# Kernel optimization log

Hardware: AMD Instinct MI355X
Metric: run time of the kernel (lower is better)

The kernel has to match this reference:

```python
import jax, jax.numpy as jnp
import numpy as np

N, IN, OUT, H = 8192, 128, 64, 4
NEG_SLOPE = 0.2   # GATConv leaky-relu slope
EPS = 1e-5        # BatchNorm1d eps
MASK_VAL = -1e9   # masked_fill value for non-edges (finite for grad safety)


def setup_inputs() -> dict:
    key = jax.random.key(0)
    ks = jax.random.split(key, 5)
    x = jax.random.normal(ks[0], (N, IN), jnp.float32)
    adj = jax.random.randint(ks[1], (N, N), 0, 2, jnp.int32)  # dense 0/1 adjacency
    W = jax.random.normal(ks[2], (H, IN, OUT), jnp.float32) * (1.0 / np.sqrt(IN))
    a_i = jax.random.normal(ks[3], (H, OUT), jnp.float32) * (1.0 / np.sqrt(OUT))
    a_j = jax.random.normal(ks[4], (H, OUT), jnp.float32) * (1.0 / np.sqrt(OUT))
    gamma = jnp.ones((H * OUT,), jnp.float32)   # BN weight
    beta = jnp.zeros((H * OUT,), jnp.float32)   # BN bias
    return {"x": x, "adj": adj, "W": W, "a_i": a_i, "a_j": a_j,
            "gamma": gamma, "beta": beta}


def reference(x, adj, W, a_i, a_j, gamma, beta):
    # --- GATConv (dense adjacency, multi-head, concat) ---
    h = jnp.einsum('ni,hio->hno', x, W)              # [H, N, OUT]
    ei = jnp.einsum('hno,ho->hn', h, a_i)            # [H, N] source scores
    ej = jnp.einsum('hno,ho->hn', h, a_j)            # [H, N] target scores
    coe = ei[:, :, None] + ej[:, None, :]            # [H, N, N]
    coe = jnp.where(coe >= 0, coe, NEG_SLOPE * coe)  # leaky_relu
    coe = jnp.where(adj[None, :, :] == 0, MASK_VAL, coe)
    att = jax.nn.softmax(coe, axis=-1)               # segment softmax over neighbors
    out = jnp.einsum('hnm,hmo->hno', att, h)         # weighted aggregation
    out = jnp.transpose(out, (1, 0, 2)).reshape(N, H * OUT)  # concat heads
    # --- BatchNorm1d (training-mode batch stats over nodes) ---
    mean = jnp.mean(out, axis=0)
    var = jnp.var(out, axis=0)
    out = (out - mean) * jax.lax.rsqrt(var + EPS) * gamma + beta
    # --- ReLU ---
    return jax.nn.relu(out)
```

## Files before the change

kernel.cpp:

```cpp
#include <hip/hip_runtime.h>
#include <hip/hip_bf16.h>

#define NN   8192
#define IND  128
#define OUTD 64
#define NH   4
#define NEG_SLOPE 0.2f
#define BN_EPS 1e-5f

typedef __attribute__((ext_vector_type(8))) short bf16x8;
typedef __attribute__((ext_vector_type(4))) float f32x4;
typedef __attribute__((ext_vector_type(4))) int   i32x4;

static __device__ __forceinline__ short f2bf(float f) {
    union { float f; unsigned u; } v; v.f = f;
    return (short)((v.u + 0x8000u) >> 16);
}

__global__ __launch_bounds__(256) void k0_repackW(const float* __restrict__ W,
                                                  short* __restrict__ WB) {
    int tid = blockIdx.x * 256 + threadIdx.x;
    int o = tid & 63, i = (tid >> 6) & 127, h = tid >> 13;
    WB[((h * 16 + (i >> 3)) * 64 + o) * 8 + (i & 7)] = f2bf(W[(h * 128 + i) * 64 + o]);
}

__global__ __launch_bounds__(256) void k1_feat(const float* __restrict__ x,
                                               const short* __restrict__ WB,
                                               const float* __restrict__ a_i,
                                               const float* __restrict__ a_j,
                                               short* __restrict__ hB,
                                               float* __restrict__ t_ei,  float* __restrict__ t_Ri,
                                               float* __restrict__ t_nj,
                                               float* __restrict__ t_E1j, float* __restrict__ t_E2j) {
    int w = threadIdx.x >> 6;
    int l = threadIdx.x & 63;
    int quad = l >> 4, lx = l & 15;
    int rb = blockIdx.x;

    f32x4 acc[4] = {};
#pragma unroll
    for (int ks = 0; ks < 4; ++ks) {
        const float* xp = x + (rb * 16 + lx) * IND + ks * 32 + quad * 8;
        f32x4 xa = *(const f32x4*)xp;
        f32x4 xb = *(const f32x4*)(xp + 4);
        bf16x8 af;
#pragma unroll
        for (int j = 0; j < 4; ++j) { af[j] = f2bf(xa[j]); af[4 + j] = f2bf(xb[j]); }
#pragma unroll
        for (int ot = 0; ot < 4; ++ot) {
            bf16x8 bf = *(const bf16x8*)(WB + ((w * 16 + ks * 4 + quad) * 64 + ot * 16 + lx) * 8);
            acc[ot] = __builtin_amdgcn_mfma_f32_16x16x32_bf16(af, bf, acc[ot], 0, 0, 0);
        }
    }
    float aiv[4], ajv[4];
#pragma unroll
    for (int ot = 0; ot < 4; ++ot) {
        aiv[ot] = a_i[w * 64 + ot * 16 + lx];
        ajv[ot] = a_j[w * 64 + ot * 16 + lx];
    }
#pragma unroll
    for (int reg = 0; reg < 4; ++reg) {
        int row = rb * 16 + quad * 4 + reg;
        float ei = 0.f, ej = 0.f;
#pragma unroll
        for (int ot = 0; ot < 4; ++ot) {
            float hv = acc[ot][reg];
            ei += hv * aiv[ot];
            ej += hv * ajv[ot];
        }
#pragma unroll
        for (int m = 1; m <= 8; m <<= 1) {
            ei += __shfl_xor(ei, m, 64);
            ej += __shfl_xor(ej, m, 64);
        }
        if (lx == reg) {
            t_ei [w * NN + row] = ei;
            t_Ri [w * NN + row] = expf(-0.8f * ei);
            t_nj [w * NN + row] = -ej;
            t_E1j[w * NN + row] = expf(ej);
            t_E2j[w * NN + row] = expf(NEG_SLOPE * ej);
        }
#pragma unroll
        for (int ot = 0; ot < 4; ++ot) {
            int o = ot * 16 + lx;
            hB[((w * 1024 + (row >> 3)) * 64 + o) * 8 + (row & 7)] = f2bf(acc[ot][reg]);
        }
    }
}

__global__ __launch_bounds__(256) void k2_attn(const int* __restrict__ adj,
                                               const short* __restrict__ hB,
                                               const float* __restrict__ t_ei,
                                               const float* __restrict__ t_Ri,
                                               const float* __restrict__ t_nj,
                                               const float* __restrict__ t_E1j,
                                               const float* __restrict__ t_E2j,
                                               float* __restrict__ num,
                                               float* __restrict__ Lsum) {
    __shared__ unsigned char smask[64 * 260];
    int tid = threadIdx.x;
    int w = tid >> 6;
    int l = tid & 63;
    int quad = l >> 4, lx = l & 15;
    int rb = blockIdx.x >> 2, ks = blockIdx.x & 3;
    int rowbase = rb * 64;
    int tb = w * NN;
    int k0 = ks * 2048;

    {
        int kc = tid * 8;
#pragma unroll 2
        for (int i = 0; i < 64; ++i) {
            const int* ap = adj + (size_t)(rowbase + i) * NN + k0 + kc;
            i32x4 a0 = *(const i32x4*)ap;
            i32x4 a1 = *(const i32x4*)(ap + 4);
            unsigned m = 0;
#pragma unroll
            for (int j = 0; j < 4; ++j) {
                m |= (a0[j] ? 1u : 0u) << j;
                m |= (a1[j] ? 1u : 0u) << (4 + j);
            }
            smask[i * 260 + tid] = (unsigned char)m;
        }
    }
    __syncthreads();

    float eiv[4], Riv[4];
    int mrow[4];
#pragma unroll
    for (int r = 0; r < 4; ++r) {
        int i = rowbase + r * 16 + lx;
        eiv[r] = t_ei[tb + i];
        Riv[r] = t_Ri[tb + i];
        mrow[r] = (r * 16 + lx) * 260 + quad;
    }

    bf16x8 onesf;
#pragma unroll
    for (int j = 0; j < 8; ++j) onesf[j] = (short)0x3F80;

    f32x4 acc[4][4] = {};
    f32x4 accL[4] = {};
    f32x4 pnj0, pnj1, pe10, pe11, pe20, pe21;
    {
        int kb = k0 + quad * 8;
        pnj0 = *(const f32x4*)(t_nj  + tb + kb);
        pnj1 = *(const f32x4*)(t_nj  + tb + kb + 4);
        pe10 = *(const f32x4*)(t_E1j + tb + kb);
        pe11 = *(const f32x4*)(t_E1j + tb + kb + 4);
        pe20 = *(const f32x4*)(t_E2j + tb + kb);
        pe21 = *(const f32x4*)(t_E2j + tb + kb + 4);
    }

#pragma unroll 1
    for (int kt = 0; kt < 64; ++kt) {
        f32x4 nj0 = pnj0, nj1 = pnj1;
        f32x4 e1j0 = pe10, e1j1 = pe11;
        f32x4 e2j0 = pe20, e2j1 = pe21;
        int mc[4];
#pragma unroll
        for (int r = 0; r < 4; ++r) mc[r] = smask[mrow[r] + kt * 4];

        int ktn = (kt + 1) & 63;
        int kbn = k0 + ktn * 32 + quad * 8;
        pnj0 = *(const f32x4*)(t_nj  + tb + kbn);
        pnj1 = *(const f32x4*)(t_nj  + tb + kbn + 4);
        pe10 = *(const f32x4*)(t_E1j + tb + kbn);
        pe11 = *(const f32x4*)(t_E1j + tb + kbn + 4);
        pe20 = *(const f32x4*)(t_E2j + tb + kbn);
        pe21 = *(const f32x4*)(t_E2j + tb + kbn + 4);

        int kb = k0 + kt * 32 + quad * 8;
        bf16x8 bfrag[4];
#pragma unroll
        for (int ot = 0; ot < 4; ++ot)
            bfrag[ot] = *(const bf16x8*)(hB + ((w * 1024 + (kb >> 3)) * 64 + ot * 16 + lx) * 8);

        bf16x8 afr[4];
#pragma unroll
        for (int r = 0; r < 4; ++r) {
            union { i32x4 i; bf16x8 b; } af;
#pragma unroll
            for (int jj = 0; jj < 4; ++jj) {
                int j0 = 2 * jj, j1 = 2 * jj + 1;
                float njA = (j0 < 4) ? nj0[j0] : nj1[j0 - 4];
                float njB = (j1 < 4) ? nj0[j1] : nj1[j1 - 4];
                float e1A = (j0 < 4) ? e1j0[j0] : e1j1[j0 - 4];
                float e1B = (j1 < 4) ? e1j0[j1] : e1j1[j1 - 4];
                float e2A = (j0 < 4) ? e2j0[j0] : e2j1[j0 - 4];
                float e2B = (j1 < 4) ? e2j0[j1] : e2j1[j1 - 4];
                float p0 = (eiv[r] >= njA) ? e1A : Riv[r] * e2A;
                float p1 = (eiv[r] >= njB) ? e1B : Riv[r] * e2B;
                p0 = (mc[r] & (1 << j0)) ? p0 : 0.0f;
                p1 = (mc[r] & (1 << j1)) ? p1 : 0.0f;
                af.i[jj] = (int)__builtin_amdgcn_perm(__float_as_uint(p1),
                                                      __float_as_uint(p0),
                                                      0x07060302);
            }
            afr[r] = af.b;
        }
#pragma unroll
        for (int r = 0; r < 4; ++r)
            accL[r] = __builtin_amdgcn_mfma_f32_16x16x32_bf16(afr[r], onesf, accL[r], 0, 0, 0);
#pragma unroll
        for (int r = 0; r < 4; ++r)
#pragma unroll
            for (int ot = 0; ot < 4; ++ot)
                acc[r][ot] = __builtin_amdgcn_mfma_f32_16x16x32_bf16(afr[r], bfrag[ot], acc[r][ot], 0, 0, 0);
    }

#pragma unroll
    for (int r = 0; r < 4; ++r)
        if (lx == 0)
#pragma unroll
            for (int reg = 0; reg < 4; ++reg)
                atomicAdd(&Lsum[w * NN + rowbase + r * 16 + quad * 4 + reg], accL[r][reg]);
#pragma unroll
    for (int r = 0; r < 4; ++r)
#pragma unroll
        for (int ot = 0; ot < 4; ++ot)
#pragma unroll
            for (int reg = 0; reg < 4; ++reg) {
                int row = rowbase + r * 16 + quad * 4 + reg;
                atomicAdd(&num[row * 256 + w * 64 + ot * 16 + lx], acc[r][ot][reg]);
            }
}

__global__ __launch_bounds__(256) void k3_combine(float* __restrict__ num,
                                                  const float* __restrict__ Lsum,
                                                  float* __restrict__ stats) {
    int c = threadIdx.x;
    int h = c >> 6;
    float s = 0.f, s2 = 0.f;
#pragma unroll
    for (int rr = 0; rr < 8; ++rr) {
        int row = blockIdx.x * 8 + rr;
        float L = Lsum[h * NN + row];
        float val = num[row * 256 + c] / L;
        num[row * 256 + c] = val;
        s += val; s2 += val * val;
    }
    atomicAdd(&stats[c], s);
    atomicAdd(&stats[c + 256], s2);
}

__global__ __launch_bounds__(256) void k5_apply(const float* __restrict__ preout,
                                                const float* __restrict__ stats,
                                                const float* __restrict__ gamma,
                                                const float* __restrict__ beta,
                                                float* __restrict__ out) {
    __shared__ float sbnp[512];
    int c = threadIdx.x;
    float mean = stats[c] * (1.0f / NN);
    float var  = stats[c + 256] * (1.0f / NN) - mean * mean;
    float sc = gamma[c] * rsqrtf(var + BN_EPS);
    sbnp[c] = sc;
    sbnp[c + 256] = beta[c] - mean * sc;
    __syncthreads();

    int g = blockIdx.x * 256 + threadIdx.x;
    f32x4 v = *(const f32x4*)(preout + (size_t)g * 4);
    int cb = (g * 4) & 255;
    f32x4 r;
#pragma unroll
    for (int j = 0; j < 4; ++j)
        r[j] = fmaxf(v[j] * sbnp[cb + j] + sbnp[256 + cb + j], 0.0f);
    *(f32x4*)(out + (size_t)g * 4) = r;
}

extern "C" void kernel_launch(void* const* d_in, const int* in_sizes, int n_in,
                              void* d_out, int out_size, void* d_ws, size_t ws_size,
                              hipStream_t stream) {
    (void)in_sizes; (void)n_in; (void)out_size; (void)ws_size;
    const float* x     = (const float*)d_in[0];
    const int*   adj   = (const int*)d_in[1];
    const float* W     = (const float*)d_in[2];
    const float* a_i   = (const float*)d_in[3];
    const float* a_j   = (const float*)d_in[4];
    const float* gamma = (const float*)d_in[5];
    const float* beta  = (const float*)d_in[6];
    float* out = (float*)d_out;

    char* ws = (char*)d_ws;
    short* WB    = (short*)(ws + 0);
    short* hB    = (short*)(ws + 65536);
    float* t_ei  = (float*)(ws + 4259840);
    float* t_Ri  = t_ei + 32768;
    float* t_nj  = t_ei + 2 * 32768;
    float* t_E1j = t_ei + 3 * 32768;
    float* t_E2j = t_ei + 4 * 32768;
    float* num   = (float*)(ws + 5046272);
    float* Lsum  = (float*)(ws + 13434880);
    float* stats = (float*)(ws + 13565952);

    hipMemsetAsync(num, 0, 8388608 + 131072 + 2048, stream);

    k0_repackW<<<dim3(128),  dim3(256), 0, stream>>>(W, WB);
    k1_feat   <<<dim3(512),  dim3(256), 0, stream>>>(x, WB, a_i, a_j, hB,
                                                     t_ei, t_Ri, t_nj, t_E1j, t_E2j);
    k2_attn   <<<dim3(512),  dim3(256), 0, stream>>>(adj, hB,
                                                     t_ei, t_Ri, t_nj, t_E1j, t_E2j,
                                                     num, Lsum);
    k3_combine<<<dim3(1024), dim3(256), 0, stream>>>(num, Lsum, stats);
    k5_apply  <<<dim3(2048), dim3(256), 0, stream>>>(num, stats, gamma, beta, out);
}
```

Baseline: 489.1 us.

## Replace leaky-relu branch with fmax, prefetch h fragments, defer normalization

```diff
diff --git a/kernel.cpp b/kernel.cpp
--- a/kernel.cpp
+++ b/kernel.cpp
@@ -29,8 +29,7 @@
                                                const float* __restrict__ a_i,
                                                const float* __restrict__ a_j,
                                                short* __restrict__ hB,
-                                               float* __restrict__ t_ei,  float* __restrict__ t_Ri,
-                                               float* __restrict__ t_nj,
+                                               float* __restrict__ t_Ri,
                                                float* __restrict__ t_E1j, float* __restrict__ t_E2j) {
     int w = threadIdx.x >> 6;
     int l = threadIdx.x & 63;
@@ -74,9 +73,7 @@
             ej += __shfl_xor(ej, m, 64);
         }
         if (lx == reg) {
-            t_ei [w * NN + row] = ei;
             t_Ri [w * NN + row] = expf(-0.8f * ei);
-            t_nj [w * NN + row] = -ej;
             t_E1j[w * NN + row] = expf(ej);
             t_E2j[w * NN + row] = expf(NEG_SLOPE * ej);
         }
@@ -90,9 +87,7 @@
 
 __global__ __launch_bounds__(256) void k2_attn(const int* __restrict__ adj,
                                                const short* __restrict__ hB,
-                                               const float* __restrict__ t_ei,
                                                const float* __restrict__ t_Ri,
-                                               const float* __restrict__ t_nj,
                                                const float* __restrict__ t_E1j,
                                                const float* __restrict__ t_E2j,
                                                float* __restrict__ num,
@@ -125,12 +120,11 @@
     }
     __syncthreads();
 
-    float eiv[4], Riv[4];
+    float Riv[4];
     int mrow[4];
 #pragma unroll
     for (int r = 0; r < 4; ++r) {
         int i = rowbase + r * 16 + lx;
-        eiv[r] = t_ei[tb + i];
         Riv[r] = t_Ri[tb + i];
         mrow[r] = (r * 16 + lx) * 260 + quad;
     }
@@ -141,40 +135,40 @@
 
     f32x4 acc[4][4] = {};
     f32x4 accL[4] = {};
-    f32x4 pnj0, pnj1, pe10, pe11, pe20, pe21;
+    f32x4 pe10, pe11, pe20, pe21;
+    bf16x8 pbf[4];
     {
         int kb = k0 + quad * 8;
-        pnj0 = *(const f32x4*)(t_nj  + tb + kb);
-        pnj1 = *(const f32x4*)(t_nj  + tb + kb + 4);
         pe10 = *(const f32x4*)(t_E1j + tb + kb);
         pe11 = *(const f32x4*)(t_E1j + tb + kb + 4);
         pe20 = *(const f32x4*)(t_E2j + tb + kb);
         pe21 = *(const f32x4*)(t_E2j + tb + kb + 4);
+#pragma unroll
+        for (int ot = 0; ot < 4; ++ot)
+            pbf[ot] = *(const bf16x8*)(hB + ((w * 1024 + (kb >> 3)) * 64 + ot * 16 + lx) * 8);
     }
 
 #pragma unroll 1
     for (int kt = 0; kt < 64; ++kt) {
-        f32x4 nj0 = pnj0, nj1 = pnj1;
         f32x4 e1j0 = pe10, e1j1 = pe11;
         f32x4 e2j0 = pe20, e2j1 = pe21;
-        int mc[4];
-#pragma unroll
-        for (int r = 0; r < 4; ++r) mc[r] = smask[mrow[r] + kt * 4];
+        bf16x8 bfrag[4];
+#pragma unroll
+        for (int ot = 0; ot < 4; ++ot) bfrag[ot] = pbf[ot];
 
         int ktn = (kt + 1) & 63;
         int kbn = k0 + ktn * 32 + quad * 8;
-        pnj0 = *(const f32x4*)(t_nj  + tb + kbn);
-        pnj1 = *(const f32x4*)(t_nj  + tb + kbn + 4);
         pe10 = *(const f32x4*)(t_E1j + tb + kbn);
         pe11 = *(const f32x4*)(t_E1j + tb + kbn + 4);
         pe20 = *(const f32x4*)(t_E2j + tb + kbn);
         pe21 = *(const f32x4*)(t_E2j + tb + kbn + 4);
-
-        int kb = k0 + kt * 32 + quad * 8;
-        bf16x8 bfrag[4];
 #pragma unroll
         for (int ot = 0; ot < 4; ++ot)
-            bfrag[ot] = *(const bf16x8*)(hB + ((w * 1024 + (kb >> 3)) * 64 + ot * 16 + lx) * 8);
+            pbf[ot] = *(const bf16x8*)(hB + ((w * 1024 + (kbn >> 3)) * 64 + ot * 16 + lx) * 8);
+
+        int mc[4];
+#pragma unroll
+        for (int r = 0; r < 4; ++r) mc[r] = smask[mrow[r] + kt * 4];
 
         bf16x8 afr[4];
 #pragma unroll
@@ -183,14 +177,12 @@
 #pragma unroll
             for (int jj = 0; jj < 4; ++jj) {
                 int j0 = 2 * jj, j1 = 2 * jj + 1;
-                float njA = (j0 < 4) ? nj0[j0] : nj1[j0 - 4];
-                float njB = (j1 < 4) ? nj0[j1] : nj1[j1 - 4];
                 float e1A = (j0 < 4) ? e1j0[j0] : e1j1[j0 - 4];
                 float e1B = (j1 < 4) ? e1j0[j1] : e1j1[j1 - 4];
                 float e2A = (j0 < 4) ? e2j0[j0] : e2j1[j0 - 4];
                 float e2B = (j1 < 4) ? e2j0[j1] : e2j1[j1 - 4];
-                float p0 = (eiv[r] >= njA) ? e1A : Riv[r] * e2A;
-                float p1 = (eiv[r] >= njB) ? e1B : Riv[r] * e2B;
+                float p0 = fmaxf(e1A, Riv[r] * e2A);
+                float p1 = fmaxf(e1B, Riv[r] * e2B);
                 p0 = (mc[r] & (1 << j0)) ? p0 : 0.0f;
                 p1 = (mc[r] & (1 << j1)) ? p1 : 0.0f;
                 af.i[jj] = (int)__builtin_amdgcn_perm(__float_as_uint(p1),
@@ -226,25 +218,24 @@
             }
 }
 
-__global__ __launch_bounds__(256) void k3_combine(float* __restrict__ num,
-                                                  const float* __restrict__ Lsum,
-                                                  float* __restrict__ stats) {
+__global__ __launch_bounds__(256) void k3_stats(const float* __restrict__ num,
+                                                const float* __restrict__ Lsum,
+                                                float* __restrict__ stats) {
     int c = threadIdx.x;
     int h = c >> 6;
     float s = 0.f, s2 = 0.f;
 #pragma unroll
     for (int rr = 0; rr < 8; ++rr) {
         int row = blockIdx.x * 8 + rr;
-        float L = Lsum[h * NN + row];
-        float val = num[row * 256 + c] / L;
-        num[row * 256 + c] = val;
+        float val = num[row * 256 + c] / Lsum[h * NN + row];
         s += val; s2 += val * val;
     }
     atomicAdd(&stats[c], s);
     atomicAdd(&stats[c + 256], s2);
 }
 
-__global__ __launch_bounds__(256) void k5_apply(const float* __restrict__ preout,
+__global__ __launch_bounds__(256) void k5_apply(const float* __restrict__ num,
+                                                const float* __restrict__ Lsum,
                                                 const float* __restrict__ stats,
                                                 const float* __restrict__ gamma,
                                                 const float* __restrict__ beta,
@@ -259,12 +250,14 @@
     __syncthreads();
 
     int g = blockIdx.x * 256 + threadIdx.x;
-    f32x4 v = *(const f32x4*)(preout + (size_t)g * 4);
+    f32x4 v = *(const f32x4*)(num + (size_t)g * 4);
     int cb = (g * 4) & 255;
+    int row = g >> 6;
+    float rL = 1.0f / Lsum[(cb >> 6) * NN + row];
     f32x4 r;
 #pragma unroll
     for (int j = 0; j < 4; ++j)
-        r[j] = fmaxf(v[j] * sbnp[cb + j] + sbnp[256 + cb + j], 0.0f);
+        r[j] = fmaxf((v[j] * rL) * sbnp[cb + j] + sbnp[256 + cb + j], 0.0f);
     *(f32x4*)(out + (size_t)g * 4) = r;
 }
 
@@ -284,23 +277,20 @@
     char* ws = (char*)d_ws;
     short* WB    = (short*)(ws + 0);
     short* hB    = (short*)(ws + 65536);
-    float* t_ei  = (float*)(ws + 4259840);
-    float* t_Ri  = t_ei + 32768;
-    float* t_nj  = t_ei + 2 * 32768;
-    float* t_E1j = t_ei + 3 * 32768;
-    float* t_E2j = t_ei + 4 * 32768;
-    float* num   = (float*)(ws + 5046272);
-    float* Lsum  = (float*)(ws + 13434880);
-    float* stats = (float*)(ws + 13565952);
+    float* t_Ri  = (float*)(ws + 4259840);
+    float* t_E1j = t_Ri + 32768;
+    float* t_E2j = t_Ri + 2 * 32768;
+    float* num   = (float*)(ws + 4784128);
+    float* Lsum  = (float*)(ws + 13172736);
+    float* stats = (float*)(ws + 13303808);
 
     hipMemsetAsync(num, 0, 8388608 + 131072 + 2048, stream);
 
     k0_repackW<<<dim3(128),  dim3(256), 0, stream>>>(W, WB);
     k1_feat   <<<dim3(512),  dim3(256), 0, stream>>>(x, WB, a_i, a_j, hB,
-                                                     t_ei, t_Ri, t_nj, t_E1j, t_E2j);
-    k2_attn   <<<dim3(512),  dim3(256), 0, stream>>>(adj, hB,
-                                                     t_ei, t_Ri, t_nj, t_E1j, t_E2j,
+                                                     t_Ri, t_E1j, t_E2j);
+    k2_attn   <<<dim3(512),  dim3(256), 0, stream>>>(adj, hB, t_Ri, t_E1j, t_E2j,
                                                      num, Lsum);
-    k3_combine<<<dim3(1024), dim3(256), 0, stream>>>(num, Lsum, stats);
-    k5_apply  <<<dim3(2048), dim3(256), 0, stream>>>(num, stats, gamma, beta, out);
-}
+    k3_stats  <<<dim3(1024), dim3(256), 0, stream>>>(num, Lsum, stats);
+    k5_apply  <<<dim3(2048), dim3(256), 0, stream>>>(num, Lsum, stats, gamma, beta, out);
+}
```

After: 481.6 us. Within noise of the previous version (-1.5%).
